# Kernel optimization log

Hardware: AMD Instinct MI355X
Metric: run time of the kernel (lower is better)

The kernel has to match this reference:

```python
import jax, jax.numpy as jnp
import numpy as np

N_HEADS = 8
IN_DIM = 128
H_DIM = 512
B, N, L = 4, 64, 256


def setup_inputs() -> dict:
    key = jax.random.key(0)
    ks = jax.random.split(key, 11)
    s = 0.02
    return {
        "query": jax.random.normal(ks[0], (B, N, L, IN_DIM), jnp.float32),
        "key": jax.random.normal(ks[1], (B, N, L, IN_DIM), jnp.float32),
        "value": jax.random.normal(ks[2], (B, N, L, IN_DIM), jnp.float32),
        "Wq": jax.random.normal(ks[3], (IN_DIM, H_DIM), jnp.float32) * s,
        "bq": jnp.zeros((H_DIM,), jnp.float32),
        "Wk": jax.random.normal(ks[4], (IN_DIM, H_DIM), jnp.float32) * s,
        "bk": jnp.zeros((H_DIM,), jnp.float32),
        "Wv": jax.random.normal(ks[5], (IN_DIM, H_DIM), jnp.float32) * s,
        "bv": jnp.zeros((H_DIM,), jnp.float32),
        "Wo": jax.random.normal(ks[6], (H_DIM, H_DIM), jnp.float32) * s,
        "bo": jnp.zeros((H_DIM,), jnp.float32),
    }


def reference(query, key, value, Wq, bq, Wk, bk, Wv, bv, Wo, bo):
    # Conv2d 1x1 over the channel dim after permute == linear along last dim.
    hd = H_DIM // N_HEADS  # head_dim
    b, n, lq, _ = query.shape
    lk = key.shape[-2]
    q = query @ Wq + bq   # (B, N, Lq, H_DIM)
    k = key @ Wk + bk     # (B, N, Lk, H_DIM)
    v = value @ Wv + bv   # (B, N, Lk, H_DIM)
    # split heads along the last dim (matches torch.split/cat head-major trick)
    q = q.reshape(b, n, lq, N_HEADS, hd)
    k = k.reshape(b, n, lk, N_HEADS, hd)
    v = v.reshape(b, n, lk, N_HEADS, hd)
    scores = jnp.einsum("bnqhd,bnkhd->bnhqk", q, k) / jnp.sqrt(jnp.float32(hd))
    attn = jax.nn.softmax(scores, axis=-1)
    out = jnp.einsum("bnhqk,bnkhd->bnqhd", attn, v).reshape(b, n, lq, H_DIM)
    return out @ Wo + bo
```

## Files before the change

### kernel.cpp

```cpp
#include <hip/hip_runtime.h>
#include <stdint.h>
#include <stddef.h>


typedef __attribute__((ext_vector_type(8))) short short8;
typedef __attribute__((ext_vector_type(4))) float f32x4;

#define AS1(p) ((const __attribute__((address_space(1))) void*)(p))
#define AS3(p) ((__attribute__((address_space(3))) void*)(p))

__device__ __forceinline__ float b2f(uint16_t u) {
    union { uint32_t i; float f; } x; x.i = ((uint32_t)u) << 16; return x.f;
}
__device__ __forceinline__ uint16_t f2b(float f) {
    union { float f; uint32_t i; } x; x.f = f;
    uint32_t r = x.i + 0x7fffu + ((x.i >> 16) & 1u);
    return (uint16_t)(r >> 16);
}

__global__ void k_detect(const uint16_t* __restrict__ q, int* __restrict__ flag) {
    const int t = threadIdx.x;
    int cnt = 0;
    for (int i = 0; i < 32; ++i) {
        const int e = (q[t * 32 + i] >> 7) & 0xff;
        cnt += (e < 110) | (e > 135);
    }
#pragma unroll
    for (int m = 1; m < 64; m <<= 1) cnt += __shfl_xor(cnt, m, 64);
    if (t == 0) *flag = (cnt > 256) ? 1 : 0;
}

__device__ __forceinline__ uint16_t rd_any(const void* p, size_t idx, int isf) {
    return isf ? f2b(((const float*)p)[idx]) : ((const uint16_t*)p)[idx];
}

__global__ void k_transpose(const void* __restrict__ Wq, const void* __restrict__ Wk,
                            const void* __restrict__ Wv, const void* __restrict__ Wo,
                            uint16_t* __restrict__ wtq, uint16_t* __restrict__ wtk,
                            uint16_t* __restrict__ wtv, uint16_t* __restrict__ wto,
                            const int* __restrict__ flag) {
    const int isf = *flag;
    const int z = blockIdx.y;
    const int t = blockIdx.x * 256 + threadIdx.x;
    if (z < 3) {
        if (t >= 128 * 512) return;
        const void* W = (z == 0) ? Wq : (z == 1) ? Wk : Wv;
        uint16_t* o = (z == 0) ? wtq : (z == 1) ? wtk : wtv;
        const int k = t & 127, n = t >> 7;
        o[t] = rd_any(W, (size_t)k * 512 + n, isf);
    } else {
        const int k = t & 511, n = t >> 9;
        wto[t] = rd_any(Wo, (size_t)k * 512 + n, isf);
    }
}

template<int KITERS>
__device__ __forceinline__ void gemm_dev(const void* __restrict__ Av, const int lda,
                                         const uint16_t* __restrict__ Wt,
                                         const void* __restrict__ biasv,
                                         void* __restrict__ Cv,
                                         const int isf_a, const int isf_bias, const int isf_c) {
    __shared__ __align__(16) uint16_t At[128 * 64];
    __shared__ __align__(16) uint16_t Bt[128 * 64];
    const int m0 = blockIdx.x * 128, n0 = blockIdx.y * 128;
    const int tid = threadIdx.x;
    const int lane = tid & 63, w = tid >> 6;
    const int wr = w >> 1, wc = w & 1;
    const int quad = lane >> 4, cl = lane & 15;

    f32x4 acc[4][4];
#pragma unroll
    for (int i = 0; i < 4; ++i)
#pragma unroll
        for (int j = 0; j < 4; ++j) acc[i][j] = (f32x4){0.f, 0.f, 0.f, 0.f};

#pragma unroll 1
    for (int kt = 0; kt < KITERS; ++kt) {
        const int k0 = kt * 64;
        __syncthreads();
        if (!isf_a) {
#pragma unroll
            for (int i = 0; i < 4; ++i) {
                const int s = i * 256 + tid;
                const int row = s >> 3;
                const int gc = (s & 7) ^ (row & 7);
                __builtin_amdgcn_global_load_lds(AS1((const uint16_t*)Av + (size_t)(m0 + row) * lda + k0 + gc * 8),
                                                 AS3(At + (size_t)(i * 256 + w * 64) * 8), 16, 0, 0);
                __builtin_amdgcn_global_load_lds(AS1(Wt + (size_t)(n0 + row) * lda + k0 + gc * 8),
                                                 AS3(Bt + (size_t)(i * 256 + w * 64) * 8), 16, 0, 0);
            }
        } else {
#pragma unroll
            for (int i = 0; i < 4; ++i) {
                const int s = i * 256 + tid;
                const int row = s >> 3;
                const int gc = (s & 7) ^ (row & 7);
                __builtin_amdgcn_global_load_lds(AS1(Wt + (size_t)(n0 + row) * lda + k0 + gc * 8),
                                                 AS3(Bt + (size_t)(i * 256 + w * 64) * 8), 16, 0, 0);
                const float* p = (const float*)Av + (size_t)(m0 + row) * lda + k0 + gc * 8;
                const f32x4 u0 = *(const f32x4*)p;
                const f32x4 u1 = *(const f32x4*)(p + 4);
                short8 tv;
#pragma unroll
                for (int j = 0; j < 4; ++j) {
                    tv[j] = (short)f2b(u0[j]);
                    tv[4 + j] = (short)f2b(u1[j]);
                }
                *(short8*)(At + (size_t)s * 8) = tv;
            }
        }
        __syncthreads();
#pragma unroll
        for (int ks = 0; ks < 2; ++ks) {
            short8 af[4], bf[4];
#pragma unroll
            for (int mt = 0; mt < 4; ++mt) {
                const int row = wr * 64 + mt * 16 + cl;
                const int slot = row * 8 + ((ks * 4 + quad) ^ (row & 7));
                af[mt] = *(const short8*)(At + slot * 8);
            }
#pragma unroll
            for (int nt = 0; nt < 4; ++nt) {
                const int row = wc * 64 + nt * 16 + cl;
                const int slot = row * 8 + ((ks * 4 + quad) ^ (row & 7));
                bf[nt] = *(const short8*)(Bt + slot * 8);
            }
#pragma unroll
            for (int mt = 0; mt < 4; ++mt)
#pragma unroll
                for (int nt = 0; nt < 4; ++nt)
                    acc[mt][nt] = __builtin_amdgcn_mfma_f32_16x16x32_bf16(af[mt], bf[nt], acc[mt][nt], 0, 0, 0);
        }
    }
#pragma unroll
    for (int nt = 0; nt < 4; ++nt) {
        const int col = n0 + wc * 64 + nt * 16 + cl;
        const float bv = isf_bias ? ((const float*)biasv)[col] : b2f(((const uint16_t*)biasv)[col]);
#pragma unroll
        for (int mt = 0; mt < 4; ++mt)
#pragma unroll
            for (int r = 0; r < 4; ++r) {
                const int rowg = m0 + wr * 64 + mt * 16 + quad * 4 + r;
                const size_t off = (size_t)rowg * 512 + col;
                const float v = acc[mt][nt][r] + bv;
                if (!isf_c) ((uint16_t*)Cv)[off] = f2b(v);
                else        ((float*)Cv)[off] = v;
            }
    }
}

__global__ __launch_bounds__(256, 2) void k_gemm_proj(
    const void* qi, const void* ki, const void* vi,
    const uint16_t* wtq, const uint16_t* wtk, const uint16_t* wtv,
    const void* bq, const void* bk, const void* bv,
    uint16_t* cq, uint16_t* ck, uint16_t* cv, const int* flag) {
    const int isf = *flag;
    const int z = blockIdx.z;
    const void* A = (z == 0) ? qi : (z == 1) ? ki : vi;
    const uint16_t* W = (z == 0) ? wtq : (z == 1) ? wtk : wtv;
    const void* B = (z == 0) ? bq : (z == 1) ? bk : bv;
    uint16_t* C = (z == 0) ? cq : (z == 1) ? ck : cv;
    gemm_dev<2>(A, 128, W, B, C, isf, isf, 0);
}

__global__ __launch_bounds__(256, 2) void k_gemm_out(
    const uint16_t* __restrict__ A, const uint16_t* __restrict__ Wt,
    const void* __restrict__ bias, void* __restrict__ C, const int* flag) {
    const int isf = *flag;
    gemm_dev<8>(A, 512, Wt, bias, C, 0, isf, isf);
}

__global__ __launch_bounds__(256, 2) void k_attn(const uint16_t* __restrict__ qws,
                                                 const uint16_t* __restrict__ kws,
                                                 const uint16_t* __restrict__ vws,
                                                 uint16_t* __restrict__ ows) {
    __shared__ __align__(16) uint16_t sm[16384];

    const int bx = blockIdx.x;
    const int bn = bx >> 3, h = bx & 7;
    const int tid = threadIdx.x;
    const int lane = tid & 63, w = tid >> 6;
    const int quad = lane >> 4, cl = lane & 15;
    const size_t base = (size_t)bn * 256 * 512 + h * 64;
    const int qbase = w * 64;

    short8 qf[4][2];
#pragma unroll
    for (int mt = 0; mt < 4; ++mt)
#pragma unroll
        for (int ks = 0; ks < 2; ++ks)
            qf[mt][ks] = *(const short8*)(qws + base + (size_t)(qbase + mt * 16 + cl) * 512 + ks * 32 + quad * 8);

    f32x4 O[4][4];
    float lsum[4];
#pragma unroll
    for (int mt = 0; mt < 4; ++mt) {
#pragma unroll
        for (int nt = 0; nt < 4; ++nt) O[mt][nt] = (f32x4){0.f, 0.f, 0.f, 0.f};
        lsum[mt] = 0.f;
    }

    short8 vreg[2];
    {
#pragma unroll
        for (int i = 0; i < 2; ++i) {
            const int s = i * 256 + tid;
            const int row = s >> 3;
            const int gc = (s & 7) ^ (row & 7);
            __builtin_amdgcn_global_load_lds(AS1(kws + base + (size_t)row * 512 + gc * 8),
                                             AS3(sm + (i * 256 + w * 64) * 8), 16, 0, 0);
        }
#pragma unroll
        for (int i = 0; i < 2; ++i) {
            const int it = i * 256 + tid;
            const int key = it >> 3, db = (it & 7) * 8;
            vreg[i] = *(const short8*)(vws + base + (size_t)key * 512 + db);
        }
#pragma unroll
        for (int i = 0; i < 2; ++i) {
            const int it = i * 256 + tid;
            const int key = it >> 3, db = (it & 7) * 8;
            const int c = ((key >> 5) & 1) * 4 + ((key >> 2) & 3);
            const int j2 = ((key >> 4) & 1) * 4 + (key & 3);
#pragma unroll
            for (int j = 0; j < 8; ++j) {
                const int d = db + j;
                const int fd = ((d >> 3) ^ d) & 7;
                sm[8192 + d * 64 + ((c ^ fd) & 7) * 8 + j2] = (uint16_t)vreg[i][j];
            }
        }
    }
    __syncthreads();

    int cur = 0;
#pragma unroll 1
    for (int kb = 0; kb < 4; ++kb) {
        const uint16_t* const Kc = sm + cur * 4096;
        const uint16_t* const Vc = sm + 8192 + cur * 4096;
        const int nb = cur ^ 1;

        if (kb < 3) {
#pragma unroll
            for (int i = 0; i < 2; ++i) {
                const int s = i * 256 + tid;
                const int row = s >> 3;
                const int gc = (s & 7) ^ (row & 7);
                __builtin_amdgcn_global_load_lds(AS1(kws + base + (size_t)((kb + 1) * 64 + row) * 512 + gc * 8),
                                                 AS3(sm + nb * 4096 + (i * 256 + w * 64) * 8), 16, 0, 0);
            }
#pragma unroll
            for (int i = 0; i < 2; ++i) {
                const int it = i * 256 + tid;
                const int key = it >> 3, db = (it & 7) * 8;
                vreg[i] = *(const short8*)(vws + base + (size_t)((kb + 1) * 64 + key) * 512 + db);
            }
        }

#pragma unroll
        for (int hf = 0; hf < 2; ++hf) {
            short8 kf[2][2];
#pragma unroll
            for (int nt2 = 0; nt2 < 2; ++nt2)
#pragma unroll
                for (int ks = 0; ks < 2; ++ks) {
                    const int row = (hf * 2 + nt2) * 16 + cl;
                    const int slot = row * 8 + ((ks * 4 + quad) ^ (row & 7));
                    kf[nt2][ks] = *(const short8*)(Kc + slot * 8);
                }
            short8 vf[4];
#pragma unroll
            for (int nt = 0; nt < 4; ++nt) {
                const int d = nt * 16 + cl;
                const int fd = ((d >> 3) ^ d) & 7;
                vf[nt] = *(const short8*)(Vc + d * 64 + (((hf * 4 + quad) ^ fd) & 7) * 8);
            }
#pragma unroll
            for (int mt = 0; mt < 4; ++mt) {
                f32x4 S0 = (f32x4){0.f, 0.f, 0.f, 0.f};
                f32x4 S1 = (f32x4){0.f, 0.f, 0.f, 0.f};
#pragma unroll
                for (int ks = 0; ks < 2; ++ks) {
                    S0 = __builtin_amdgcn_mfma_f32_16x16x32_bf16(kf[0][ks], qf[mt][ks], S0, 0, 0, 0);
                    S1 = __builtin_amdgcn_mfma_f32_16x16x32_bf16(kf[1][ks], qf[mt][ks], S1, 0, 0, 0);
                }
                short8 pf;
                float ls = 0.f;
#pragma unroll
                for (int r = 0; r < 4; ++r) {
                    const float pv = __expf(S0[r] * 0.125f);
                    ls += pv;
                    pf[r] = (short)f2b(pv);
                }
#pragma unroll
                for (int r = 0; r < 4; ++r) {
                    const float pv = __expf(S1[r] * 0.125f);
                    ls += pv;
                    pf[4 + r] = (short)f2b(pv);
                }
                lsum[mt] += ls;
#pragma unroll
                for (int nt = 0; nt < 4; ++nt)
                    O[mt][nt] = __builtin_amdgcn_mfma_f32_16x16x32_bf16(pf, vf[nt], O[mt][nt], 0, 0, 0);
            }
        }

        if (kb < 3) {
#pragma unroll
            for (int i = 0; i < 2; ++i) {
                const int it = i * 256 + tid;
                const int key = it >> 3, db = (it & 7) * 8;
                const int c = ((key >> 5) & 1) * 4 + ((key >> 2) & 3);
                const int j2 = ((key >> 4) & 1) * 4 + (key & 3);
#pragma unroll
                for (int j = 0; j < 8; ++j) {
                    const int d = db + j;
                    const int fd = ((d >> 3) ^ d) & 7;
                    sm[8192 + nb * 4096 + d * 64 + ((c ^ fd) & 7) * 8 + j2] = (uint16_t)vreg[i][j];
                }
            }
        }
        __syncthreads();
        cur = nb;
    }

    float linv[4];
#pragma unroll
    for (int mt = 0; mt < 4; ++mt) {
        float v = lsum[mt];
        v += __shfl_xor(v, 16, 64);
        v += __shfl_xor(v, 32, 64);
        linv[mt] = 1.0f / v;
    }

    uint16_t* const Ob = sm + w * 4096;
#pragma unroll
    for (int mt = 0; mt < 4; ++mt) {
        float ln4[4];
#pragma unroll
        for (int r = 0; r < 4; ++r) ln4[r] = __shfl(linv[mt], quad * 4 + r, 64);
#pragma unroll
        for (int nt = 0; nt < 4; ++nt)
#pragma unroll
            for (int r = 0; r < 4; ++r) {
                const int row = mt * 16 + quad * 4 + r;
                const int col = nt * 16 + cl;
                Ob[row * 64 + ((((col >> 3) ^ (row & 7)) & 7) * 8 + (col & 7))] =
                    f2b(O[mt][nt][r] * ln4[r]);
            }
    }
#pragma unroll
    for (int g = 0; g < 8; ++g) {
        const int row = g * 8 + (lane >> 3);
        const int c = lane & 7;
        const short8 ov = *(const short8*)(Ob + row * 64 + ((c ^ (row & 7)) & 7) * 8);
        *(short8*)(ows + base + (size_t)(qbase + row) * 512 + c * 8) = ov;
    }
}

extern "C" void kernel_launch(void* const* d_in, const int* in_sizes, int n_in,
                              void* d_out, int out_size, void* d_ws, size_t ws_size,
                              hipStream_t stream) {
    uint16_t* ws = (uint16_t*)d_ws;

    int* flag = (int*)d_ws;
    uint16_t* wt_q = ws + 256;
    uint16_t* wt_k = wt_q + 128 * 512;
    uint16_t* wt_v = wt_k + 128 * 512;
    uint16_t* wt_o = wt_v + 128 * 512;
    uint16_t* q_ws = wt_o + 512 * 512;
    const size_t QKV = (size_t)65536 * 512;
    uint16_t* k_ws = q_ws + QKV;
    uint16_t* v_ws = k_ws + QKV;

    k_detect<<<1, 64, 0, stream>>>((const uint16_t*)d_in[0], flag);
    k_transpose<<<dim3(1024, 4), 256, 0, stream>>>(d_in[3], d_in[5], d_in[7], d_in[9],
                                                   wt_q, wt_k, wt_v, wt_o, flag);
    k_gemm_proj<<<dim3(512, 4, 3), 256, 0, stream>>>(d_in[0], d_in[1], d_in[2],
                                                     wt_q, wt_k, wt_v,
                                                     d_in[4], d_in[6], d_in[8],
                                                     q_ws, k_ws, v_ws, flag);
    k_attn<<<dim3(2048), 256, 0, stream>>>(q_ws, k_ws, v_ws, q_ws);
    k_gemm_out<<<dim3(512, 4), 256, 0, stream>>>(q_ws, wt_o, d_in[10], d_out, flag);
}
```

Baseline: 455.4 us.

## Use 128-wide K tiles, swap grid order, and stage bf16 epilogue through LDS

Doubles the GEMM K-tile from 64 to 128, halving the number of K iterations and barrier pairs per tile, with a swizzle that covers 16 column chunks. The grid axes are swapped so the four N-blocks sharing the same A rows run next to each other, which should improve L2 reuse of the activations. The bf16 output epilogue now goes through LDS so each lane writes 16-byte coalesced rows instead of scattered 2-byte stores. LDS use grows to 64 KB per block, which may limit occupancy under launch_bounds(256,2).

```diff
diff --git a/kernel.cpp b/kernel.cpp
--- a/kernel.cpp
+++ b/kernel.cpp
@@ -60,9 +60,9 @@
                                          const void* __restrict__ biasv,
                                          void* __restrict__ Cv,
                                          const int isf_a, const int isf_bias, const int isf_c) {
-    __shared__ __align__(16) uint16_t At[128 * 64];
-    __shared__ __align__(16) uint16_t Bt[128 * 64];
-    const int m0 = blockIdx.x * 128, n0 = blockIdx.y * 128;
+    __shared__ __align__(16) uint16_t smA[128 * 128];
+    __shared__ __align__(16) uint16_t smB[128 * 128];
+    const int n0 = blockIdx.x * 128, m0 = blockIdx.y * 128;
     const int tid = threadIdx.x;
     const int lane = tid & 63, w = tid >> 6;
     const int wr = w >> 1, wc = w & 1;
@@ -76,27 +76,20 @@
 
 #pragma unroll 1
     for (int kt = 0; kt < KITERS; ++kt) {
-        const int k0 = kt * 64;
+        const int k0 = kt * 128;
         __syncthreads();
-        if (!isf_a) {
-#pragma unroll
-            for (int i = 0; i < 4; ++i) {
-                const int s = i * 256 + tid;
-                const int row = s >> 3;
-                const int gc = (s & 7) ^ (row & 7);
+#pragma unroll
+        for (int i = 0; i < 8; ++i) {
+            const int s = i * 256 + tid;
+            const int row = s >> 4;
+            const int sc = s & 15;
+            const int gc = (sc & 8) | ((sc & 7) ^ (row & 7));
+            __builtin_amdgcn_global_load_lds(AS1(Wt + (size_t)(n0 + row) * lda + k0 + gc * 8),
+                                             AS3(smB + (size_t)(i * 256 + w * 64) * 8), 16, 0, 0);
+            if (!isf_a) {
                 __builtin_amdgcn_global_load_lds(AS1((const uint16_t*)Av + (size_t)(m0 + row) * lda + k0 + gc * 8),
-                                                 AS3(At + (size_t)(i * 256 + w * 64) * 8), 16, 0, 0);
-                __builtin_amdgcn_global_load_lds(AS1(Wt + (size_t)(n0 + row) * lda + k0 + gc * 8),
-                                                 AS3(Bt + (size_t)(i * 256 + w * 64) * 8), 16, 0, 0);
-            }
-        } else {
-#pragma unroll
-            for (int i = 0; i < 4; ++i) {
-                const int s = i * 256 + tid;
-                const int row = s >> 3;
-                const int gc = (s & 7) ^ (row & 7);
-                __builtin_amdgcn_global_load_lds(AS1(Wt + (size_t)(n0 + row) * lda + k0 + gc * 8),
-                                                 AS3(Bt + (size_t)(i * 256 + w * 64) * 8), 16, 0, 0);
+                                                 AS3(smA + (size_t)(i * 256 + w * 64) * 8), 16, 0, 0);
+            } else {
                 const float* p = (const float*)Av + (size_t)(m0 + row) * lda + k0 + gc * 8;
                 const f32x4 u0 = *(const f32x4*)p;
                 const f32x4 u1 = *(const f32x4*)(p + 4);
@@ -106,24 +99,26 @@
                     tv[j] = (short)f2b(u0[j]);
                     tv[4 + j] = (short)f2b(u1[j]);
                 }
-                *(short8*)(At + (size_t)s * 8) = tv;
+                *(short8*)(smA + (size_t)s * 8) = tv;
             }
         }
         __syncthreads();
 #pragma unroll
-        for (int ks = 0; ks < 2; ++ks) {
+        for (int ks = 0; ks < 4; ++ks) {
             short8 af[4], bf[4];
 #pragma unroll
             for (int mt = 0; mt < 4; ++mt) {
                 const int row = wr * 64 + mt * 16 + cl;
-                const int slot = row * 8 + ((ks * 4 + quad) ^ (row & 7));
-                af[mt] = *(const short8*)(At + slot * 8);
+                const int q = ks * 4 + quad;
+                const int sc = (q & 8) | ((q & 7) ^ (row & 7));
+                af[mt] = *(const short8*)(smA + (row * 16 + sc) * 8);
             }
 #pragma unroll
             for (int nt = 0; nt < 4; ++nt) {
                 const int row = wc * 64 + nt * 16 + cl;
-                const int slot = row * 8 + ((ks * 4 + quad) ^ (row & 7));
-                bf[nt] = *(const short8*)(Bt + slot * 8);
+                const int q = ks * 4 + quad;
+                const int sc = (q & 8) | ((q & 7) ^ (row & 7));
+                bf[nt] = *(const short8*)(smB + (row * 16 + sc) * 8);
             }
 #pragma unroll
             for (int mt = 0; mt < 4; ++mt)
@@ -132,20 +127,43 @@
                     acc[mt][nt] = __builtin_amdgcn_mfma_f32_16x16x32_bf16(af[mt], bf[nt], acc[mt][nt], 0, 0, 0);
         }
     }
-#pragma unroll
-    for (int nt = 0; nt < 4; ++nt) {
-        const int col = n0 + wc * 64 + nt * 16 + cl;
-        const float bv = isf_bias ? ((const float*)biasv)[col] : b2f(((const uint16_t*)biasv)[col]);
-#pragma unroll
-        for (int mt = 0; mt < 4; ++mt)
-#pragma unroll
-            for (int r = 0; r < 4; ++r) {
-                const int rowg = m0 + wr * 64 + mt * 16 + quad * 4 + r;
-                const size_t off = (size_t)rowg * 512 + col;
-                const float v = acc[mt][nt][r] + bv;
-                if (!isf_c) ((uint16_t*)Cv)[off] = f2b(v);
-                else        ((float*)Cv)[off] = v;
-            }
+    if (!isf_c) {
+        __syncthreads();
+        uint16_t* const Ob = smA + w * 4096;
+#pragma unroll
+        for (int nt = 0; nt < 4; ++nt) {
+            const int col = nt * 16 + cl;
+            const float bv = isf_bias ? ((const float*)biasv)[n0 + wc * 64 + col]
+                                      : b2f(((const uint16_t*)biasv)[n0 + wc * 64 + col]);
+#pragma unroll
+            for (int mt = 0; mt < 4; ++mt)
+#pragma unroll
+                for (int r = 0; r < 4; ++r) {
+                    const int row = mt * 16 + quad * 4 + r;
+                    Ob[row * 64 + (((col >> 3) ^ (row & 7)) & 7) * 8 + (col & 7)] =
+                        f2b(acc[mt][nt][r] + bv);
+                }
+        }
+#pragma unroll
+        for (int g = 0; g < 8; ++g) {
+            const int row = g * 8 + (lane >> 3);
+            const int c = lane & 7;
+            const short8 ov = *(const short8*)(Ob + row * 64 + ((c ^ (row & 7)) & 7) * 8);
+            *(short8*)((uint16_t*)Cv + (size_t)(m0 + wr * 64 + row) * 512 + n0 + wc * 64 + c * 8) = ov;
+        }
+    } else {
+#pragma unroll
+        for (int nt = 0; nt < 4; ++nt) {
+            const int col = n0 + wc * 64 + nt * 16 + cl;
+            const float bv = isf_bias ? ((const float*)biasv)[col] : b2f(((const uint16_t*)biasv)[col]);
+#pragma unroll
+            for (int mt = 0; mt < 4; ++mt)
+#pragma unroll
+                for (int r = 0; r < 4; ++r) {
+                    const int rowg = m0 + wr * 64 + mt * 16 + quad * 4 + r;
+                    ((float*)Cv)[(size_t)rowg * 512 + col] = acc[mt][nt][r] + bv;
+                }
+        }
     }
 }
 
@@ -160,14 +178,14 @@
     const uint16_t* W = (z == 0) ? wtq : (z == 1) ? wtk : wtv;
     const void* B = (z == 0) ? bq : (z == 1) ? bk : bv;
     uint16_t* C = (z == 0) ? cq : (z == 1) ? ck : cv;
-    gemm_dev<2>(A, 128, W, B, C, isf, isf, 0);
+    gemm_dev<1>(A, 128, W, B, C, isf, isf, 0);
 }
 
 __global__ __launch_bounds__(256, 2) void k_gemm_out(
     const uint16_t* __restrict__ A, const uint16_t* __restrict__ Wt,
     const void* __restrict__ bias, void* __restrict__ C, const int* flag) {
     const int isf = *flag;
-    gemm_dev<8>(A, 512, Wt, bias, C, 0, isf, isf);
+    gemm_dev<4>(A, 512, Wt, bias, C, 0, isf, isf);
 }
 
 __global__ __launch_bounds__(256, 2) void k_attn(const uint16_t* __restrict__ qws,
@@ -375,10 +393,10 @@
     k_detect<<<1, 64, 0, stream>>>((const uint16_t*)d_in[0], flag);
     k_transpose<<<dim3(1024, 4), 256, 0, stream>>>(d_in[3], d_in[5], d_in[7], d_in[9],
                                                    wt_q, wt_k, wt_v, wt_o, flag);
-    k_gemm_proj<<<dim3(512, 4, 3), 256, 0, stream>>>(d_in[0], d_in[1], d_in[2],
+    k_gemm_proj<<<dim3(4, 512, 3), 256, 0, stream>>>(d_in[0], d_in[1], d_in[2],
                                                      wt_q, wt_k, wt_v,
                                                      d_in[4], d_in[6], d_in[8],
                                                      q_ws, k_ws, v_ws, flag);
     k_attn<<<dim3(2048), 256, 0, stream>>>(q_ws, k_ws, v_ws, q_ws);
-    k_gemm_out<<<dim3(512, 4), 256, 0, stream>>>(q_ws, wt_o, d_in[10], d_out, flag);
-}
+    k_gemm_out<<<dim3(4, 512), 256, 0, stream>>>(q_ws, wt_o, d_in[10], d_out, flag);
+}
```

Measured after the change: 476.5 us. 1.05x slower.

## Stage GEMM bf16 epilogue through LDS and remap blocks for XCD locality

Applied to the files above, without the earlier changes.

The bf16 output path of the shared GEMM routine now writes biased results into swizzled LDS tiles, then emits 16-byte vector stores per row instead of scattered 2-byte stores. Block indices in both GEMM kernels are remapped so consecutive hardware blocks (assigned round-robin to XCDs) place all four column tiles of a row tile on the same XCD, improving L2 reuse of the A rows. This adds an extra barrier and LDS round trip in the epilogue and index arithmetic per block.

```diff
diff --git a/kernel.cpp b/kernel.cpp
--- a/kernel.cpp
+++ b/kernel.cpp
@@ -59,10 +59,10 @@
                                          const uint16_t* __restrict__ Wt,
                                          const void* __restrict__ biasv,
                                          void* __restrict__ Cv,
+                                         const int m0, const int n0,
                                          const int isf_a, const int isf_bias, const int isf_c) {
     __shared__ __align__(16) uint16_t At[128 * 64];
     __shared__ __align__(16) uint16_t Bt[128 * 64];
-    const int m0 = blockIdx.x * 128, n0 = blockIdx.y * 128;
     const int tid = threadIdx.x;
     const int lane = tid & 63, w = tid >> 6;
     const int wr = w >> 1, wc = w & 1;
@@ -132,20 +132,43 @@
                     acc[mt][nt] = __builtin_amdgcn_mfma_f32_16x16x32_bf16(af[mt], bf[nt], acc[mt][nt], 0, 0, 0);
         }
     }
-#pragma unroll
-    for (int nt = 0; nt < 4; ++nt) {
-        const int col = n0 + wc * 64 + nt * 16 + cl;
-        const float bv = isf_bias ? ((const float*)biasv)[col] : b2f(((const uint16_t*)biasv)[col]);
-#pragma unroll
-        for (int mt = 0; mt < 4; ++mt)
-#pragma unroll
-            for (int r = 0; r < 4; ++r) {
-                const int rowg = m0 + wr * 64 + mt * 16 + quad * 4 + r;
-                const size_t off = (size_t)rowg * 512 + col;
-                const float v = acc[mt][nt][r] + bv;
-                if (!isf_c) ((uint16_t*)Cv)[off] = f2b(v);
-                else        ((float*)Cv)[off] = v;
-            }
+    if (!isf_c) {
+        __syncthreads();
+        uint16_t* const Ob = ((w & 2) ? Bt : At) + (w & 1) * 4096;
+#pragma unroll
+        for (int nt = 0; nt < 4; ++nt) {
+            const int col = nt * 16 + cl;
+            const float bv = isf_bias ? ((const float*)biasv)[n0 + wc * 64 + col]
+                                      : b2f(((const uint16_t*)biasv)[n0 + wc * 64 + col]);
+#pragma unroll
+            for (int mt = 0; mt < 4; ++mt)
+#pragma unroll
+                for (int r = 0; r < 4; ++r) {
+                    const int row = mt * 16 + quad * 4 + r;
+                    Ob[row * 64 + (((col >> 3) ^ (row & 7)) & 7) * 8 + (col & 7)] =
+                        f2b(acc[mt][nt][r] + bv);
+                }
+        }
+#pragma unroll
+        for (int g = 0; g < 8; ++g) {
+            const int row = g * 8 + (lane >> 3);
+            const int c = lane & 7;
+            const short8 ov = *(const short8*)(Ob + row * 64 + ((c ^ (row & 7)) & 7) * 8);
+            *(short8*)((uint16_t*)Cv + (size_t)(m0 + wr * 64 + row) * 512 + n0 + wc * 64 + c * 8) = ov;
+        }
+    } else {
+#pragma unroll
+        for (int nt = 0; nt < 4; ++nt) {
+            const int col = n0 + wc * 64 + nt * 16 + cl;
+            const float bv = isf_bias ? ((const float*)biasv)[col] : b2f(((const uint16_t*)biasv)[col]);
+#pragma unroll
+            for (int mt = 0; mt < 4; ++mt)
+#pragma unroll
+                for (int r = 0; r < 4; ++r) {
+                    const int rowg = m0 + wr * 64 + mt * 16 + quad * 4 + r;
+                    ((float*)Cv)[(size_t)rowg * 512 + col] = acc[mt][nt][r] + bv;
+                }
+        }
     }
 }
 
@@ -155,19 +178,27 @@
     const void* bq, const void* bk, const void* bv,
     uint16_t* cq, uint16_t* ck, uint16_t* cv, const int* flag) {
     const int isf = *flag;
-    const int z = blockIdx.z;
+    const int id = blockIdx.x + (blockIdx.y << 2) + (blockIdx.z << 11);
+    const int nid = (id & 7) * 768 + (id >> 3);
+    const int z = nid >> 11;
+    const int y = (nid >> 2) & 511;
+    const int x = nid & 3;
     const void* A = (z == 0) ? qi : (z == 1) ? ki : vi;
     const uint16_t* W = (z == 0) ? wtq : (z == 1) ? wtk : wtv;
     const void* B = (z == 0) ? bq : (z == 1) ? bk : bv;
     uint16_t* C = (z == 0) ? cq : (z == 1) ? ck : cv;
-    gemm_dev<2>(A, 128, W, B, C, isf, isf, 0);
+    gemm_dev<2>(A, 128, W, B, C, y * 128, x * 128, isf, isf, 0);
 }
 
 __global__ __launch_bounds__(256, 2) void k_gemm_out(
     const uint16_t* __restrict__ A, const uint16_t* __restrict__ Wt,
     const void* __restrict__ bias, void* __restrict__ C, const int* flag) {
     const int isf = *flag;
-    gemm_dev<8>(A, 512, Wt, bias, C, 0, isf, isf);
+    const int id = blockIdx.x + (blockIdx.y << 2);
+    const int nid = (id & 7) * 256 + (id >> 3);
+    const int y = nid >> 2;
+    const int x = nid & 3;
+    gemm_dev<8>(A, 512, Wt, bias, C, y * 128, x * 128, 0, isf, isf);
 }
 
 __global__ __launch_bounds__(256, 2) void k_attn(const uint16_t* __restrict__ qws,
@@ -375,10 +406,10 @@
     k_detect<<<1, 64, 0, stream>>>((const uint16_t*)d_in[0], flag);
     k_transpose<<<dim3(1024, 4), 256, 0, stream>>>(d_in[3], d_in[5], d_in[7], d_in[9],
                                                    wt_q, wt_k, wt_v, wt_o, flag);
-    k_gemm_proj<<<dim3(512, 4, 3), 256, 0, stream>>>(d_in[0], d_in[1], d_in[2],
+    k_gemm_proj<<<dim3(4, 512, 3), 256, 0, stream>>>(d_in[0], d_in[1], d_in[2],
                                                      wt_q, wt_k, wt_v,
                                                      d_in[4], d_in[6], d_in[8],
                                                      q_ws, k_ws, v_ws, flag);
     k_attn<<<dim3(2048), 256, 0, stream>>>(q_ws, k_ws, v_ws, q_ws);
-    k_gemm_out<<<dim3(512, 4), 256, 0, stream>>>(q_ws, wt_o, d_in[10], d_out, flag);
-}
+    k_gemm_out<<<dim3(4, 512), 256, 0, stream>>>(q_ws, wt_o, d_in[10], d_out, flag);
+}
```

After: 428.6 us. -5.9%, faster.
